# Performance work log

Hardware: AMD Instinct MI355X
Metric: run time of the kernel (lower is better)

Reference implementation:

```python
import jax, jax.numpy as jnp
import numpy as np

# static config (matches init_kwargs)
STRIDE, PAD, DIL, DG = 1, 1, 1, 1
KH, KW = 3, 3
CIN, COUT = 64, 64


def setup_inputs() -> dict:
    key = jax.random.key(0)
    k1, k2, k3, k4 = jax.random.split(key, 4)
    N, C, H, W = 4, CIN, 128, 128
    K = KH * KW
    x = jax.random.normal(k1, (N, C, H, W), dtype=jnp.float32)
    offset = jax.random.normal(k2, (N, 2 * DG * K, H, W), dtype=jnp.float32)
    mask = jax.random.uniform(k3, (N, DG * K, H, W), dtype=jnp.float32)
    stdv = 1.0 / np.sqrt(C * K)
    weight = jax.random.uniform(k4, (COUT, C, KH, KW), dtype=jnp.float32,
                                minval=-stdv, maxval=stdv)
    bias = jnp.zeros((COUT,), dtype=jnp.float32)  # no_bias=True -> frozen zeros
    return {"x": x, "offset": offset, "mask": mask, "weight": weight, "bias": bias}


def _dcnv2(x, offset, mask, weight, bias):
    N, C, H, W = x.shape
    Cout, _, kh, kw = weight.shape
    K = kh * kw
    Ho = (H + 2 * PAD - DIL * (kh - 1) - 1) // STRIDE + 1
    Wo = (W + 2 * PAD - DIL * (kw - 1) - 1) // STRIDE + 1
    Cg = C // DG

    # offsets: [N, DG, K, 2(y,x), Ho, Wo]; mask: [N, DG, K, Ho, Wo]
    off = offset.reshape(N, DG, K, 2, Ho, Wo)
    off_y, off_x = off[:, :, :, 0], off[:, :, :, 1]
    m = mask.reshape(N, DG, K, Ho, Wo)

    kidx = jnp.arange(K)
    ky, kx = kidx // kw, kidx % kw
    base_y = (jnp.arange(Ho) * STRIDE - PAD)[None, :] + (ky * DIL)[:, None]  # [K,Ho]
    base_x = (jnp.arange(Wo) * STRIDE - PAD)[None, :] + (kx * DIL)[:, None]  # [K,Wo]

    py = base_y[None, None, :, :, None].astype(x.dtype) + off_y  # [N,DG,K,Ho,Wo]
    px = base_x[None, None, :, None, :].astype(x.dtype) + off_x

    y0 = jnp.floor(py)
    x0 = jnp.floor(px)
    ly = py - y0  # frac weights
    lx = px - x0
    y0i = y0.astype(jnp.int32)
    x0i = x0.astype(jnp.int32)

    xf = x.reshape(N, DG, Cg, H * W)

    def gather(yi, xi):
        # per-corner zero padding (out-of-bounds corners contribute 0)
        valid = ((yi >= 0) & (yi < H) & (xi >= 0) & (xi < W))
        idx = jnp.clip(yi, 0, H - 1) * W + jnp.clip(xi, 0, W - 1)  # [N,DG,K,Ho,Wo]
        idx_b = jnp.broadcast_to(idx[:, :, None], (N, DG, Cg, K, Ho, Wo))
        v = jnp.take_along_axis(xf, idx_b.reshape(N, DG, Cg, -1), axis=3)
        v = v.reshape(N, DG, Cg, K, Ho, Wo)
        return v * valid[:, :, None].astype(x.dtype)

    w00 = ((1 - ly) * (1 - lx))[:, :, None]  # [N,DG,1,K,Ho,Wo]
    w01 = ((1 - ly) * lx)[:, :, None]
    w10 = (ly * (1 - lx))[:, :, None]
    w11 = (ly * lx)[:, :, None]

    val = (gather(y0i, x0i) * w00 + gather(y0i, x0i + 1) * w01
           + gather(y0i + 1, x0i) * w10 + gather(y0i + 1, x0i + 1) * w11)
    cols = val * m[:, :, None]                      # modulation
    cols = cols.reshape(N, C, K, Ho, Wo)            # DG*Cg -> C (contiguous)

    wmat = weight.reshape(Cout, C, K)
    out = jnp.einsum('nckhw,ock->nohw', cols, wmat)
    return out + bias[None, :, None, None]


def reference(x, offset, mask, weight, bias):
    return _dcnv2(x, offset, mask, weight, bias)
```

## Files before the change

kernel.cpp:

```cpp
#include <hip/hip_runtime.h>

#define N_    4
#define C_    64
#define H_    128
#define W_    128
#define KW_   3
#define K_    9
#define COUT_ 64
#define HW_   (H_ * W_)
#define NPIX  (N_ * HW_)
#define KK_   (C_ * K_)

typedef short v8s __attribute__((ext_vector_type(8)));
typedef float v4f __attribute__((ext_vector_type(4)));
typedef int   v4i __attribute__((ext_vector_type(4)));
typedef unsigned int u32;
typedef unsigned short u16;
typedef unsigned int v2u __attribute__((ext_vector_type(2)));

static __device__ __forceinline__ u16 f2bf(float f) {
    union { float f; unsigned int u; } v; v.f = f;
    unsigned int r = v.u + 0x7FFFu + ((v.u >> 16) & 1u);
    return (u16)(r >> 16);
}
static __device__ __forceinline__ u32 cvtpk(float lo, float hi) {
    u32 r;
    asm("v_cvt_pk_bf16_f32 %0, %1, %2" : "=v"(r) : "v"(lo), "v"(hi));
    return r;
}

__global__ __launch_bounds__(256) void prep(
    const float* __restrict__ x, float* __restrict__ xh,
    const float* __restrict__ w, u16* __restrict__ wA3)
{
    if (blockIdx.x < 1024) {
        const int n   = blockIdx.x >> 8;
        const int hw0 = (blockIdx.x & 255) * 64;

        __shared__ float tile[64][65];
        const float* xb = x + n * (C_ * HW_);
#pragma unroll
        for (int i = 0; i < 4; ++i) {
            const int idx = i * 256 + threadIdx.x;
            const int q   = idx & 15;
            const int c   = idx >> 4;
            const v4f v = *(const v4f*)&xb[c * HW_ + hw0 + 4 * q];
            tile[4 * q + 0][c] = v.x;
            tile[4 * q + 1][c] = v.y;
            tile[4 * q + 2][c] = v.z;
            tile[4 * q + 3][c] = v.w;
        }
        __syncthreads();
        float* xo = xh + ((size_t)n * HW_ + hw0) * 64;
#pragma unroll
        for (int i = 0; i < 4; ++i) {
            const int idx = i * 256 + threadIdx.x;
            const int c4  = idx & 15;
            const int hr  = idx >> 4;
            v4f v;
            v.x = tile[hr][4 * c4 + 0];
            v.y = tile[hr][4 * c4 + 1];
            v.z = tile[hr][4 * c4 + 2];
            v.w = tile[hr][4 * c4 + 3];
            *(v4f*)&xo[hr * 64 + 4 * c4] = v;
        }
    } else {
        const int tid = (blockIdx.x - 1024) * 256 + threadIdx.x;
        if (tid < COUT_ * KK_) {
            const int k   = tid % KK_;
            const int o   = tid / KK_;
            const int c   = k & 63;
            const int tap = k >> 6;
            wA3[tid] = f2bf(w[o * (C_ * K_) + c * K_ + tap]);
        }
    }
}

__global__ __launch_bounds__(256, 2) void dcn_fused(
    const float* __restrict__ xh,
    const float* __restrict__ offset,
    const float* __restrict__ mask,
    const u16* __restrict__ wA3,
    const float* __restrict__ bias,
    float* __restrict__ out)
{
    const int tid  = threadIdx.x;
    const int lane = tid & 63;
    const int wv   = tid >> 6;
    const int quad = lane >> 4;
    const int l16  = lane & 15;

    const int lb  = (blockIdx.x & 7) * 128 + (blockIdx.x >> 3);
    const int pxb = lb * 64;
    const int n   = pxb >> 14;
    const int hwb = pxb & (HW_ - 1);

    __shared__ float cw[576][4];
    __shared__ int   ci[576][4];
    __shared__ u16   Bt[2][64][72];

#pragma unroll
    for (int r = 0; r < 3; ++r) {
        const int e = tid + 256 * r;
        if (e < 576) {
            const int p  = e / 9;
            const int t  = e - p * 9;
            const int hw = hwb + p;
            const int ho = hw >> 7;
            const int wo = hw & (W_ - 1);
            const int ky = t / KW_;
            const int kx = t - ky * KW_;

            const float offy = offset[n * (2 * K_ * HW_) + (2 * t + 0) * HW_ + hw];
            const float offx = offset[n * (2 * K_ * HW_) + (2 * t + 1) * HW_ + hw];
            const float mval = mask[n * (K_ * HW_) + t * HW_ + hw];

            const float py = (float)(ho - 1 + ky) + offy;
            const float qx = (float)(wo - 1 + kx) + offx;
            const float y0f = floorf(py), x0f = floorf(qx);
            const float ly = py - y0f, lx = qx - x0f;
            const int y0 = (int)y0f, x0 = (int)x0f;
            const int y1 = y0 + 1,   x1 = x0 + 1;
            const bool vy0 = (y0 >= 0) & (y0 < H_);
            const bool vy1 = (y1 >= 0) & (y1 < H_);
            const bool vx0 = (x0 >= 0) & (x0 < W_);
            const bool vx1 = (x1 >= 0) & (x1 < W_);
            const int cy0 = min(max(y0, 0), H_ - 1);
            const int cy1 = min(max(y1, 0), H_ - 1);
            const int cx0 = min(max(x0, 0), W_ - 1);
            const int cx1 = min(max(x1, 0), W_ - 1);

            float* q = &cw[e][0];
            q[0] = (1.f - ly) * (1.f - lx) * mval * ((vy0 && vx0) ? 1.f : 0.f);
            q[1] = (1.f - ly) * lx         * mval * ((vy0 && vx1) ? 1.f : 0.f);
            q[2] = ly         * (1.f - lx) * mval * ((vy1 && vx0) ? 1.f : 0.f);
            q[3] = ly         * lx         * mval * ((vy1 && vx1) ? 1.f : 0.f);
            int* qi = &ci[e][0];
            qi[0] = cy0 * W_ + cx0;
            qi[1] = cy0 * W_ + cx1;
            qi[2] = cy1 * W_ + cx0;
            qi[3] = cy1 * W_ + cx1;
        }
    }
    __syncthreads();

    const float* xb4 = xh + ((size_t)n * HW_) * 64 + 4 * l16;

    const int mb   = (wv & 1) * 32;
    const int pxwl = (wv >> 1) * 32;

    v4f acc[2][2];
#pragma unroll
    for (int mh = 0; mh < 2; ++mh)
#pragma unroll
        for (int nh = 0; nh < 2; ++nh)
            acc[mh][nh] = (v4f){0.f, 0.f, 0.f, 0.f};

    v4f LA[4][4], LB[4][4];

#define ISSUE(t, R)                                                         \
    {                                                                       \
        _Pragma("unroll")                                                   \
        for (int i = 0; i < 4; ++i) {                                       \
            const int p = wv * 16 + 4 * i + quad;                           \
            const v4i o = *(const v4i*)&ci[p * 9 + (t)][0];                 \
            R[i][0] = *(const v4f*)(xb4 + (size_t)o.x * 64);                \
            R[i][1] = *(const v4f*)(xb4 + (size_t)o.y * 64);                \
            R[i][2] = *(const v4f*)(xb4 + (size_t)o.z * 64);                \
            R[i][3] = *(const v4f*)(xb4 + (size_t)o.w * 64);                \
        }                                                                   \
    }

#define FINISH(t, R, b)                                                     \
    {                                                                       \
        _Pragma("unroll")                                                   \
        for (int i = 0; i < 4; ++i) {                                       \
            const int p = wv * 16 + 4 * i + quad;                           \
            const v4f f = *(const v4f*)&cw[p * 9 + (t)][0];                 \
            float r0 = fmaf(f.x, R[i][0].x, fmaf(f.y, R[i][1].x,            \
                       fmaf(f.z, R[i][2].x, f.w * R[i][3].x)));             \
            float r1 = fmaf(f.x, R[i][0].y, fmaf(f.y, R[i][1].y,            \
                       fmaf(f.z, R[i][2].y, f.w * R[i][3].y)));             \
            float r2 = fmaf(f.x, R[i][0].z, fmaf(f.y, R[i][1].z,            \
                       fmaf(f.z, R[i][2].z, f.w * R[i][3].z)));             \
            float r3 = fmaf(f.x, R[i][0].w, fmaf(f.y, R[i][1].w,            \
                       fmaf(f.z, R[i][2].w, f.w * R[i][3].w)));             \
            v2u pk;                                                         \
            pk.x = cvtpk(r0, r1);                                           \
            pk.y = cvtpk(r2, r3);                                           \
            *(v2u*)&Bt[b][p][4 * l16] = pk;                                 \
        }                                                                   \
    }

    ISSUE(0, LA)
    ISSUE(1, LB)
    FINISH(0, LA, 0)
    __syncthreads();

#pragma unroll
    for (int t = 0; t < K_; ++t) {
        const int buf = t & 1;
        if ((t & 1) == 0) {
            if (t + 2 < K_) ISSUE(t + 2, LA)
        } else {
            if (t + 2 < K_) ISSUE(t + 2, LB)
        }

#pragma unroll
        for (int kc = 0; kc < 2; ++kc) {
            v8s bfr[2];
#pragma unroll
            for (int nh = 0; nh < 2; ++nh)
                bfr[nh] = *(const v8s*)&Bt[buf][pxwl + nh * 16 + l16][kc * 32 + quad * 8];
            v8s afr[2];
#pragma unroll
            for (int mh = 0; mh < 2; ++mh)
                afr[mh] = *(const v8s*)(wA3 + (size_t)(mb + mh * 16 + l16) * KK_
                                            + t * 64 + kc * 32 + quad * 8);
#pragma unroll
            for (int mh = 0; mh < 2; ++mh)
#pragma unroll
                for (int nh = 0; nh < 2; ++nh)
                    acc[mh][nh] = __builtin_amdgcn_mfma_f32_16x16x32_bf16(
                        afr[mh], bfr[nh], acc[mh][nh], 0, 0, 0);
        }

        if ((t & 1) == 0) {
            if (t + 1 < K_) FINISH(t + 1, LB, buf ^ 1)
        } else {
            if (t + 1 < K_) FINISH(t + 1, LA, buf ^ 1)
        }
        __syncthreads();
    }
#undef ISSUE
#undef FINISH

    float* outb = out + n * (COUT_ * HW_);
#pragma unroll
    for (int mh = 0; mh < 2; ++mh)
#pragma unroll
        for (int nh = 0; nh < 2; ++nh)
#pragma unroll
            for (int r = 0; r < 4; ++r) {
                const int m = mb + mh * 16 + quad * 4 + r;
                outb[m * HW_ + hwb + pxwl + nh * 16 + l16] = acc[mh][nh][r] + bias[m];
            }
}

__global__ __launch_bounds__(256) void dcn_fallback(
    const float* __restrict__ x, const float* __restrict__ offset,
    const float* __restrict__ mask, const float* __restrict__ wptr,
    const float* __restrict__ bias, float* __restrict__ out)
{
    const int pix = blockIdx.x * 256 + threadIdx.x;
    const int n = pix >> 14, hw = pix & (HW_ - 1);
    const int ho = hw >> 7,  wo = hw & (W_ - 1);
    float acc[COUT_];
#pragma unroll
    for (int o = 0; o < COUT_; ++o) acc[o] = bias[o];
    const float* xn   = x + n * (C_ * HW_);
    const float* offn = offset + n * (2 * K_ * HW_) + hw;
    const float* mn   = mask + n * (K_ * HW_) + hw;
    for (int ct = 0; ct < C_; ct += 8) {
        for (int k = 0; k < K_; ++k) {
            const int ky = k / KW_, kx = k - ky * KW_;
            const float off_y = offn[(2 * k + 0) * HW_];
            const float off_x = offn[(2 * k + 1) * HW_];
            const float m = mn[k * HW_];
            const float py = (float)(ho - 1 + ky) + off_y;
            const float px = (float)(wo - 1 + kx) + off_x;
            const float y0f = floorf(py), x0f = floorf(px);
            const float ly = py - y0f, lx = px - x0f;
            const int y0 = (int)y0f, x0 = (int)x0f, y1 = y0 + 1, x1 = x0 + 1;
            const bool vy0 = (y0 >= 0) & (y0 < H_), vy1 = (y1 >= 0) & (y1 < H_);
            const bool vx0 = (x0 >= 0) & (x0 < W_), vx1 = (x1 >= 0) & (x1 < W_);
            const int cy0 = min(max(y0, 0), H_ - 1), cy1 = min(max(y1, 0), H_ - 1);
            const int cx0 = min(max(x0, 0), W_ - 1), cx1 = min(max(x1, 0), W_ - 1);
            const int i00 = cy0 * W_ + cx0, i01 = cy0 * W_ + cx1;
            const int i10 = cy1 * W_ + cx0, i11 = cy1 * W_ + cx1;
            const float f00 = (1.f - ly) * (1.f - lx) * m * ((vy0 && vx0) ? 1.f : 0.f);
            const float f01 = (1.f - ly) * lx * m * ((vy0 && vx1) ? 1.f : 0.f);
            const float f10 = ly * (1.f - lx) * m * ((vy1 && vx0) ? 1.f : 0.f);
            const float f11 = ly * lx * m * ((vy1 && vx1) ? 1.f : 0.f);
            for (int cc = 0; cc < 8; ++cc) {
                const int c = ct + cc;
                const float* xc = xn + c * HW_;
                const float val = fmaf(f00, xc[i00], fmaf(f01, xc[i01],
                                  fmaf(f10, xc[i10], f11 * xc[i11])));
#pragma unroll
                for (int o = 0; o < COUT_; ++o)
                    acc[o] = fmaf(wptr[o * (C_ * K_) + c * K_ + k], val, acc[o]);
            }
        }
    }
    float* outp = out + n * (COUT_ * HW_) + hw;
#pragma unroll
    for (int o = 0; o < COUT_; ++o) outp[o * HW_] = acc[o];
}

extern "C" void kernel_launch(void* const* d_in, const int* in_sizes, int n_in,
                              void* d_out, int out_size, void* d_ws, size_t ws_size,
                              hipStream_t stream) {
    const float* x      = (const float*)d_in[0];
    const float* offset = (const float*)d_in[1];
    const float* mask   = (const float*)d_in[2];
    const float* weight = (const float*)d_in[3];
    const float* bias   = (const float*)d_in[4];
    float* out = (float*)d_out;

    const size_t xh_bytes = (size_t)NPIX * C_ * sizeof(float);
    const size_t wA_bytes = (size_t)COUT_ * KK_ * sizeof(u16);

    if (ws_size >= xh_bytes + wA_bytes) {
        float* xh  = (float*)d_ws;
        u16*   wA3 = (u16*)((char*)d_ws + xh_bytes);
        prep<<<1024 + 144, 256, 0, stream>>>(x, xh, weight, wA3);
        dcn_fused<<<NPIX / 64, 256, 0, stream>>>(xh, offset, mask, wA3, bias, out);
    } else {
        dcn_fallback<<<NPIX / 256, 256, 0, stream>>>(x, offset, mask, weight, bias, out);
    }
}
```

Measured before the change: 119.7 us.

## Store transposed input and weights in fp16 and interpolate with packed half math

Converts the NHWC staging copy of x and the weight matrix from fp32/bf16 to fp16, which halves the bytes moved by each bilinear gather. Interpolation coefficients are kept in fp16 and the four-corner blend is done with packed half FMAs on 8-channel vectors, feeding fp16 MFMA instead of bf16. It also raises the launch-bounds occupancy target from 2 to 4 blocks per CU. The cost is lower-precision arithmetic in the interpolation, fp16 range limits, and tighter register pressure.

```diff
diff --git a/kernel.cpp b/kernel.cpp
--- a/kernel.cpp
+++ b/kernel.cpp
@@ -11,27 +11,15 @@
 #define NPIX  (N_ * HW_)
 #define KK_   (C_ * K_)
 
-typedef short v8s __attribute__((ext_vector_type(8)));
+typedef _Float16 h2 __attribute__((ext_vector_type(2)));
+typedef _Float16 h4 __attribute__((ext_vector_type(4)));
+typedef _Float16 h8 __attribute__((ext_vector_type(8)));
 typedef float v4f __attribute__((ext_vector_type(4)));
 typedef int   v4i __attribute__((ext_vector_type(4)));
-typedef unsigned int u32;
-typedef unsigned short u16;
-typedef unsigned int v2u __attribute__((ext_vector_type(2)));
-
-static __device__ __forceinline__ u16 f2bf(float f) {
-    union { float f; unsigned int u; } v; v.f = f;
-    unsigned int r = v.u + 0x7FFFu + ((v.u >> 16) & 1u);
-    return (u16)(r >> 16);
-}
-static __device__ __forceinline__ u32 cvtpk(float lo, float hi) {
-    u32 r;
-    asm("v_cvt_pk_bf16_f32 %0, %1, %2" : "=v"(r) : "v"(lo), "v"(hi));
-    return r;
-}
 
 __global__ __launch_bounds__(256) void prep(
-    const float* __restrict__ x, float* __restrict__ xh,
-    const float* __restrict__ w, u16* __restrict__ wA3)
+    const float* __restrict__ x, _Float16* __restrict__ xh,
+    const float* __restrict__ w, _Float16* __restrict__ wA3)
 {
     if (blockIdx.x < 1024) {
         const int n   = blockIdx.x >> 8;
@@ -51,18 +39,18 @@
             tile[4 * q + 3][c] = v.w;
         }
         __syncthreads();
-        float* xo = xh + ((size_t)n * HW_ + hw0) * 64;
+        _Float16* xo = xh + ((size_t)n * HW_ + hw0) * 64;
 #pragma unroll
         for (int i = 0; i < 4; ++i) {
             const int idx = i * 256 + threadIdx.x;
             const int c4  = idx & 15;
             const int hr  = idx >> 4;
-            v4f v;
-            v.x = tile[hr][4 * c4 + 0];
-            v.y = tile[hr][4 * c4 + 1];
-            v.z = tile[hr][4 * c4 + 2];
-            v.w = tile[hr][4 * c4 + 3];
-            *(v4f*)&xo[hr * 64 + 4 * c4] = v;
+            h4 v;
+            v.x = (_Float16)tile[hr][4 * c4 + 0];
+            v.y = (_Float16)tile[hr][4 * c4 + 1];
+            v.z = (_Float16)tile[hr][4 * c4 + 2];
+            v.w = (_Float16)tile[hr][4 * c4 + 3];
+            *(h4*)&xo[hr * 64 + 4 * c4] = v;
         }
     } else {
         const int tid = (blockIdx.x - 1024) * 256 + threadIdx.x;
@@ -71,16 +59,16 @@
             const int o   = tid / KK_;
             const int c   = k & 63;
             const int tap = k >> 6;
-            wA3[tid] = f2bf(w[o * (C_ * K_) + c * K_ + tap]);
+            wA3[tid] = (_Float16)w[o * (C_ * K_) + c * K_ + tap];
         }
     }
 }
 
-__global__ __launch_bounds__(256, 2) void dcn_fused(
-    const float* __restrict__ xh,
+__global__ __launch_bounds__(256, 4) void dcn_fused(
+    const _Float16* __restrict__ xh,
     const float* __restrict__ offset,
     const float* __restrict__ mask,
-    const u16* __restrict__ wA3,
+    const _Float16* __restrict__ wA3,
     const float* __restrict__ bias,
     float* __restrict__ out)
 {
@@ -89,15 +77,17 @@
     const int wv   = tid >> 6;
     const int quad = lane >> 4;
     const int l16  = lane & 15;
+    const int g    = lane >> 3;
+    const int l8   = lane & 7;
 
     const int lb  = (blockIdx.x & 7) * 128 + (blockIdx.x >> 3);
     const int pxb = lb * 64;
     const int n   = pxb >> 14;
     const int hwb = pxb & (HW_ - 1);
 
-    __shared__ float cw[576][4];
-    __shared__ int   ci[576][4];
-    __shared__ u16   Bt[2][64][72];
+    __shared__ _Float16 cwh[576][4];
+    __shared__ int      ci[576][4];
+    __shared__ _Float16 Bt[2][64][72];
 
 #pragma unroll
     for (int r = 0; r < 3; ++r) {
@@ -130,11 +120,12 @@
             const int cx0 = min(max(x0, 0), W_ - 1);
             const int cx1 = min(max(x1, 0), W_ - 1);
 
-            float* q = &cw[e][0];
-            q[0] = (1.f - ly) * (1.f - lx) * mval * ((vy0 && vx0) ? 1.f : 0.f);
-            q[1] = (1.f - ly) * lx         * mval * ((vy0 && vx1) ? 1.f : 0.f);
-            q[2] = ly         * (1.f - lx) * mval * ((vy1 && vx0) ? 1.f : 0.f);
-            q[3] = ly         * lx         * mval * ((vy1 && vx1) ? 1.f : 0.f);
+            h4 q;
+            q.x = (_Float16)((1.f - ly) * (1.f - lx) * mval * ((vy0 && vx0) ? 1.f : 0.f));
+            q.y = (_Float16)((1.f - ly) * lx         * mval * ((vy0 && vx1) ? 1.f : 0.f));
+            q.z = (_Float16)(ly         * (1.f - lx) * mval * ((vy1 && vx0) ? 1.f : 0.f));
+            q.w = (_Float16)(ly         * lx         * mval * ((vy1 && vx1) ? 1.f : 0.f));
+            *(h4*)&cwh[e][0] = q;
             int* qi = &ci[e][0];
             qi[0] = cy0 * W_ + cx0;
             qi[1] = cy0 * W_ + cx1;
@@ -144,7 +135,9 @@
     }
     __syncthreads();
 
-    const float* xb4 = xh + ((size_t)n * HW_) * 64 + 4 * l16;
+    const _Float16* xb8 = xh + ((size_t)n * HW_) * 64 + 8 * l8;
+    const int pg  = wv * 16 + g;
+    const int pg8 = pg + 8;
 
     const int mb   = (wv & 1) * 32;
     const int pxwl = (wv >> 1) * 32;
@@ -156,39 +149,37 @@
         for (int nh = 0; nh < 2; ++nh)
             acc[mh][nh] = (v4f){0.f, 0.f, 0.f, 0.f};
 
-    v4f LA[4][4], LB[4][4];
+    h8 LA[2][4], LB[2][4];
 
 #define ISSUE(t, R)                                                         \
     {                                                                       \
-        _Pragma("unroll")                                                   \
-        for (int i = 0; i < 4; ++i) {                                       \
-            const int p = wv * 16 + 4 * i + quad;                           \
-            const v4i o = *(const v4i*)&ci[p * 9 + (t)][0];                 \
-            R[i][0] = *(const v4f*)(xb4 + (size_t)o.x * 64);                \
-            R[i][1] = *(const v4f*)(xb4 + (size_t)o.y * 64);                \
-            R[i][2] = *(const v4f*)(xb4 + (size_t)o.z * 64);                \
-            R[i][3] = *(const v4f*)(xb4 + (size_t)o.w * 64);                \
-        }                                                                   \
+        const v4i oa = *(const v4i*)&ci[pg  * 9 + (t)][0];                  \
+        const v4i ob = *(const v4i*)&ci[pg8 * 9 + (t)][0];                  \
+        R[0][0] = *(const h8*)(xb8 + (size_t)oa.x * 64);                    \
+        R[0][1] = *(const h8*)(xb8 + (size_t)oa.y * 64);                    \
+        R[0][2] = *(const h8*)(xb8 + (size_t)oa.z * 64);                    \
+        R[0][3] = *(const h8*)(xb8 + (size_t)oa.w * 64);                    \
+        R[1][0] = *(const h8*)(xb8 + (size_t)ob.x * 64);                    \
+        R[1][1] = *(const h8*)(xb8 + (size_t)ob.y * 64);                    \
+        R[1][2] = *(const h8*)(xb8 + (size_t)ob.z * 64);                    \
+        R[1][3] = *(const h8*)(xb8 + (size_t)ob.w * 64);                    \
     }
 
 #define FINISH(t, R, b)                                                     \
     {                                                                       \
         _Pragma("unroll")                                                   \
-        for (int i = 0; i < 4; ++i) {                                       \
-            const int p = wv * 16 + 4 * i + quad;                           \
-            const v4f f = *(const v4f*)&cw[p * 9 + (t)][0];                 \
-            float r0 = fmaf(f.x, R[i][0].x, fmaf(f.y, R[i][1].x,            \
-                       fmaf(f.z, R[i][2].x, f.w * R[i][3].x)));             \
-            float r1 = fmaf(f.x, R[i][0].y, fmaf(f.y, R[i][1].y,            \
-                       fmaf(f.z, R[i][2].y, f.w * R[i][3].y)));             \
-            float r2 = fmaf(f.x, R[i][0].z, fmaf(f.y, R[i][1].z,            \
-                       fmaf(f.z, R[i][2].z, f.w * R[i][3].z)));             \
-            float r3 = fmaf(f.x, R[i][0].w, fmaf(f.y, R[i][1].w,            \
-                       fmaf(f.z, R[i][2].w, f.w * R[i][3].w)));             \
-            v2u pk;                                                         \
-            pk.x = cvtpk(r0, r1);                                           \
-            pk.y = cvtpk(r2, r3);                                           \
-            *(v2u*)&Bt[b][p][4 * l16] = pk;                                 \
+        for (int h = 0; h < 2; ++h) {                                       \
+            const int p = wv * 16 + h * 8 + g;                              \
+            const h4 f = *(const h4*)&cwh[p * 9 + (t)][0];                  \
+            const h8 F0 = {f.x, f.x, f.x, f.x, f.x, f.x, f.x, f.x};         \
+            const h8 F1 = {f.y, f.y, f.y, f.y, f.y, f.y, f.y, f.y};         \
+            const h8 F2 = {f.z, f.z, f.z, f.z, f.z, f.z, f.z, f.z};         \
+            const h8 F3 = {f.w, f.w, f.w, f.w, f.w, f.w, f.w, f.w};         \
+            h8 rr = F0 * R[h][0];                                           \
+            rr = __builtin_elementwise_fma(F1, R[h][1], rr);                \
+            rr = __builtin_elementwise_fma(F2, R[h][2], rr);                \
+            rr = __builtin_elementwise_fma(F3, R[h][3], rr);                \
+            *(h8*)&Bt[b][p][8 * l8] = rr;                                   \
         }                                                                   \
     }
 
@@ -208,20 +199,20 @@
 
 #pragma unroll
         for (int kc = 0; kc < 2; ++kc) {
-            v8s bfr[2];
+            h8 bfr[2];
 #pragma unroll
             for (int nh = 0; nh < 2; ++nh)
-                bfr[nh] = *(const v8s*)&Bt[buf][pxwl + nh * 16 + l16][kc * 32 + quad * 8];
-            v8s afr[2];
+                bfr[nh] = *(const h8*)&Bt[buf][pxwl + nh * 16 + l16][kc * 32 + quad * 8];
+            h8 afr[2];
 #pragma unroll
             for (int mh = 0; mh < 2; ++mh)
-                afr[mh] = *(const v8s*)(wA3 + (size_t)(mb + mh * 16 + l16) * KK_
+                afr[mh] = *(const h8*)(wA3 + (size_t)(mb + mh * 16 + l16) * KK_
                                             + t * 64 + kc * 32 + quad * 8);
 #pragma unroll
             for (int mh = 0; mh < 2; ++mh)
 #pragma unroll
                 for (int nh = 0; nh < 2; ++nh)
-                    acc[mh][nh] = __builtin_amdgcn_mfma_f32_16x16x32_bf16(
+                    acc[mh][nh] = __builtin_amdgcn_mfma_f32_16x16x32_f16(
                         afr[mh], bfr[nh], acc[mh][nh], 0, 0, 0);
         }
 
@@ -308,12 +299,12 @@
     const float* bias   = (const float*)d_in[4];
     float* out = (float*)d_out;
 
-    const size_t xh_bytes = (size_t)NPIX * C_ * sizeof(float);
-    const size_t wA_bytes = (size_t)COUT_ * KK_ * sizeof(u16);
+    const size_t xh_bytes = (size_t)NPIX * C_ * sizeof(_Float16);
+    const size_t wA_bytes = (size_t)COUT_ * KK_ * sizeof(_Float16);
 
     if (ws_size >= xh_bytes + wA_bytes) {
-        float* xh  = (float*)d_ws;
-        u16*   wA3 = (u16*)((char*)d_ws + xh_bytes);
+        _Float16* xh  = (_Float16*)d_ws;
+        _Float16* wA3 = (_Float16*)((char*)d_ws + xh_bytes);
         prep<<<1024 + 144, 256, 0, stream>>>(x, xh, weight, wA3);
         dcn_fused<<<NPIX / 64, 256, 0, stream>>>(xh, offset, mask, wA3, bias, out);
     } else {
```

After: 109.6 us. -8.5%, faster.
